# Kernel tuning notes

Hardware: AMD Instinct MI355X
Metric: run time of the kernel (lower is better)

The kernel has to match this reference:

```python
import jax, jax.numpy as jnp
import numpy as np

BN_EPS = 1e-5


def _posit_intervals():
    # Replicates conditions_l1 / conditions_g1 interval tables (128 steps each).
    l1, g1 = [], []
    for e in range(16):
        for j in range(8):
            if j == 0:
                l1.append((0.0, 1.0625 / 2**16, 1.0 / 2**16))
            else:
                lo = (1.0625 + 0.125 * (j - 1)) / 2 ** (16 - e)
                hi = (1.0625 + 0.125 * j) / 2 ** (16 - e)
                l1.append((lo, hi, 0.5 * (lo + hi)))
            lo = (1.0625 + 0.125 * (j - 1)) * 2 ** e
            hi = (1.0625 + 0.125 * j) * 2 ** e
            g1.append((lo, hi, 0.5 * (lo + hi)))  # note: j==8 branch in torch code is dead
    return l1, g1

_L1, _G1 = _posit_intervals()


def posit_quantize(x):
    # Faithful emulation of the 128 sequential torch.where passes.
    ax = jnp.abs(x)          # conditions are fixed from the ORIGINAL tensor
    neg = x < 0
    y = x
    for (lo1, hi1, m1), (log_, hig, mg) in zip(_L1, _G1):
        c1 = jnp.logical_and(ax > lo1, ax < hi1)
        cg = jnp.logical_and(ax > log_, ax < hig)
        v1 = jnp.where(neg, -m1, m1).astype(x.dtype)
        vg = jnp.where(neg, -mg, mg).astype(x.dtype)
        # |y| < 1 gate uses the CURRENT tensor, as in the torch loop
        y = jnp.where(jnp.abs(y) < 1, jnp.where(c1, v1, y), jnp.where(cg, vg, y))
    return y


def conv1x1(x, w, b):
    # x: [N,C,D,H,W], w: [O,C] (kernel_size=1), b: [O]
    return jnp.einsum('ncdhw,oc->nodhw', x, w) + b[None, :, None, None, None]


def batchnorm(x, gamma, beta, mean, var):
    inv = gamma / jnp.sqrt(var + BN_EPS)
    return x * inv[None, :, None, None, None] + (beta - mean * inv)[None, :, None, None, None]


def setup_inputs() -> dict:
    key = jax.random.key(0)
    ks = jax.random.split(key, 12)
    C = 256
    x = jax.random.normal(ks[0], (8, C, 16, 32, 32), dtype=jnp.float32)
    w1 = jax.random.normal(ks[1], (C, C), dtype=jnp.float32) * 0.05
    b1 = jax.random.normal(ks[2], (C,), dtype=jnp.float32) * 0.05
    w2 = jax.random.normal(ks[3], (C, C), dtype=jnp.float32) * 0.05
    b2 = jax.random.normal(ks[4], (C,), dtype=jnp.float32) * 0.05
    g1 = jax.random.uniform(ks[5], (C,)) + 0.5
    be1 = jax.random.normal(ks[6], (C,)) * 0.1
    m1 = jax.random.normal(ks[7], (C,)) * 0.1
    v1 = jax.random.uniform(ks[8], (C,)) + 0.5
    g2 = jax.random.uniform(ks[9], (C,)) + 0.5
    be2 = jax.random.normal(ks[10], (C,)) * 0.1
    m2 = jax.random.normal(ks[11], (C,)) * 0.1
    v2 = jax.random.uniform(jax.random.fold_in(key, 99), (C,)) + 0.5
    return {"x": x, "w1": w1, "b1": b1, "g1": g1, "be1": be1, "m1": m1, "v1": v1,
            "w2": w2, "b2": b2, "g2": g2, "be2": be2, "m2": m2, "v2": v2}


def reference(x, w1, b1, g1, be1, m1, v1, w2, b2, g2, be2, m2, v2):
    residual = x
    out = conv1x1(posit_quantize(x), posit_quantize(w1), b1)
    out = jax.nn.relu(batchnorm(out, g1, be1, m1, v1))
    out = conv1x1(posit_quantize(out), posit_quantize(w2), b2)
    out = batchnorm(out, g2, be2, m2, v2)
    return jax.nn.relu(out + residual)
```

## Files before the change

### kernel.cpp

```cpp
#include <hip/hip_runtime.h>

typedef __attribute__((ext_vector_type(8))) short short8;
typedef __attribute__((ext_vector_type(4))) short s4v;
typedef __attribute__((ext_vector_type(4))) float floatx4;

#define SPOS 16384

__device__ __forceinline__ unsigned short f2bf(float f) {
    unsigned u = __float_as_uint(f);
    u += 0x7fffu + ((u >> 16) & 1u);
    return (unsigned short)(u >> 16);
}

__device__ __forceinline__ float posit_q(float x) {
    unsigned xu  = __float_as_uint(x);
    unsigned sgn = xu & 0x80000000u;
    unsigned au  = xu & 0x7fffffffu;
    unsigned m   = au & 0x007fffffu;
    unsigned r   = (au + 0x00080000u) & 0xfff00000u;
    bool bdry = (m & 0x000fffffu) == 0x00080000u;
    unsigned res;
    if (au >= 0x3f800000u) {
        res = r;
        if (m > 0x00700000u && m < 0x00780000u && au < 0x47700000u)
            res = (au & 0xff800000u) + 0x00800000u;
        if ((bdry && m != 0x00780000u) || au >= 0x47780000u)
            res = au;
    } else {
        res = (m <= 0x00080000u || m >= 0x00780000u || bdry) ? au : r;
        if (au < 0x37880000u) res = au ? 0x37800000u : 0u;
    }
    return __uint_as_float(sgn | res);
}

__global__ __launch_bounds__(256) void prep_kernel(
    const float* __restrict__ w1, const float* __restrict__ w2,
    const float* __restrict__ b1, const float* __restrict__ g1,
    const float* __restrict__ be1, const float* __restrict__ m1,
    const float* __restrict__ v1,
    const float* __restrict__ b2, const float* __restrict__ g2,
    const float* __restrict__ be2, const float* __restrict__ m2,
    const float* __restrict__ v2,
    unsigned short* __restrict__ w1q, unsigned short* __restrict__ w2q,
    float* __restrict__ cst)
{
    int i = blockIdx.x * 256 + threadIdx.x;
    if (i < 65536) {
        w1q[i] = f2bf(posit_q(w1[i]));
        w2q[i] = f2bf(posit_q(w2[i]));
        if (i < 256) {
            float inv1 = g1[i] / sqrtf(v1[i] + 1e-5f);
            cst[i]       = inv1;
            cst[256 + i] = fmaf(b1[i], inv1, be1[i] - m1[i] * inv1);
            float inv2 = g2[i] / sqrtf(v2[i] + 1e-5f);
            cst[512 + i] = inv2;
            cst[768 + i] = fmaf(b2[i], inv2, be2[i] - m2[i] * inv2);
        }
    }
}

__device__ __forceinline__ int qidx(int p, int cb) {
    return p * 256 + ((cb ^ (p & 31)) << 3);
}

__global__ __launch_bounds__(256, 4) void fused_kernel(
    const float* __restrict__ x,
    const unsigned short* __restrict__ w1q,
    const unsigned short* __restrict__ w2q,
    const float* __restrict__ cst,
    float* __restrict__ out)
{
    __shared__ alignas(16) unsigned short q[64 * 256];
    __shared__ alignas(16) float xs[4 * 512];

    const int b  = blockIdx.x;
    const int n  = b >> 8;
    const int s0 = (b & 255) << 6;
    const float* xb = x   + (size_t)n * (256 * SPOS) + s0;
    float*       ob = out + (size_t)n * (256 * SPOS) + s0;

    const int t    = threadIdx.x;
    const int lane = t & 63;
    const int w    = t >> 6;
    const int quad = lane >> 4;
    const int l15  = lane & 15;

    {
        const int g  = lane & 15;
        const int co = lane >> 4;
        float* xsw = xs + w * 512;
        const float* src0 = xb + (size_t)(64 * w + co) * SPOS + 4 * g;
        #pragma unroll
        for (int r = 0; r < 8; ++r) {
            const float4 v0 = *(const float4*)(src0 + (size_t)(8 * r) * SPOS);
            const float4 v1 = *(const float4*)(src0 + (size_t)(8 * r + 4) * SPOS);
            *(float4*)&xsw[co * 64 + ((4 * g) ^ (4 * co))]             = v0;
            *(float4*)&xsw[(co + 4) * 64 + ((4 * g) ^ (4 * (co + 4)))] = v1;
            short8 pk;
            #pragma unroll
            for (int c8 = 0; c8 < 8; ++c8)
                pk[c8] = (short)f2bf(posit_q(xsw[c8 * 64 + (lane ^ (4 * c8))]));
            *(short8*)&q[qidx(lane, 8 * w + r)] = pk;
        }
    }
    __syncthreads();

    const int mbase = w * 64;
    floatx4 acc[4][4];
    #pragma unroll
    for (int i = 0; i < 4; ++i)
        #pragma unroll
        for (int jj = 0; jj < 4; ++jj)
            acc[i][jj] = (floatx4)0.0f;

    #pragma unroll
    for (int kk = 0; kk < 256; kk += 32) {
        short8 af[4], bf[4];
        #pragma unroll
        for (int i = 0; i < 4; ++i)
            af[i] = *(const short8*)&w1q[(size_t)(mbase + 16 * i + l15) * 256 + kk + quad * 8];
        #pragma unroll
        for (int jj = 0; jj < 4; ++jj)
            bf[jj] = *(const short8*)&q[qidx(16 * jj + l15, (kk >> 3) + quad)];
        #pragma unroll
        for (int i = 0; i < 4; ++i)
            #pragma unroll
            for (int jj = 0; jj < 4; ++jj)
                acc[i][jj] = __builtin_amdgcn_mfma_f32_16x16x32_bf16(af[i], bf[jj], acc[i][jj], 0, 0, 0);
    }
    __syncthreads();

    {
        const float* sc1 = cst;
        const float* bi1 = cst + 256;
        #pragma unroll
        for (int i = 0; i < 4; ++i) {
            const int m0 = mbase + 16 * i + quad * 4;
            float sc[4], bi[4];
            #pragma unroll
            for (int r = 0; r < 4; ++r) { sc[r] = sc1[m0 + r]; bi[r] = bi1[m0 + r]; }
            #pragma unroll
            for (int jj = 0; jj < 4; ++jj) {
                const int p = 16 * jj + l15;
                s4v h;
                #pragma unroll
                for (int r = 0; r < 4; ++r) {
                    float z = fmaf(acc[i][jj][r], sc[r], bi[r]);
                    z = fmaxf(z, 0.0f);
                    h[r] = (short)f2bf(posit_q(z));
                }
                *(s4v*)&q[qidx(p, m0 >> 3) + (m0 & 7)] = h;
            }
        }
    }
    __syncthreads();

    #pragma unroll
    for (int i = 0; i < 4; ++i)
        #pragma unroll
        for (int jj = 0; jj < 4; ++jj)
            acc[i][jj] = (floatx4)0.0f;

    #pragma unroll
    for (int kk = 0; kk < 256; kk += 32) {
        short8 af[4], bf[4];
        #pragma unroll
        for (int i = 0; i < 4; ++i)
            af[i] = *(const short8*)&w2q[(size_t)(mbase + 16 * i + l15) * 256 + kk + quad * 8];
        #pragma unroll
        for (int jj = 0; jj < 4; ++jj)
            bf[jj] = *(const short8*)&q[qidx(16 * jj + l15, (kk >> 3) + quad)];
        #pragma unroll
        for (int i = 0; i < 4; ++i)
            #pragma unroll
            for (int jj = 0; jj < 4; ++jj)
                acc[i][jj] = __builtin_amdgcn_mfma_f32_16x16x32_bf16(af[i], bf[jj], acc[i][jj], 0, 0, 0);
    }

    {
        const float* sc2 = cst + 512;
        const float* bi2 = cst + 768;
        #pragma unroll
        for (int i = 0; i < 4; ++i) {
            const int m0 = mbase + 16 * i + quad * 4;
            float sc[4], bi[4];
            #pragma unroll
            for (int r = 0; r < 4; ++r) { sc[r] = sc2[m0 + r]; bi[r] = bi2[m0 + r]; }
            #pragma unroll
            for (int jj = 0; jj < 4; ++jj) {
                const int p = 16 * jj + l15;
                #pragma unroll
                for (int r = 0; r < 4; ++r) {
                    const size_t off = (size_t)(m0 + r) * SPOS + p;
                    float v = fmaf(acc[i][jj][r], sc[r], bi[r]);
                    v += xb[off];
                    ob[off] = fmaxf(v, 0.0f);
                }
            }
        }
    }
}

extern "C" void kernel_launch(void* const* d_in, const int* in_sizes, int n_in,
                              void* d_out, int out_size, void* d_ws, size_t ws_size,
                              hipStream_t stream) {
    const float* x   = (const float*)d_in[0];
    const float* w1  = (const float*)d_in[1];
    const float* b1  = (const float*)d_in[2];
    const float* g1  = (const float*)d_in[3];
    const float* be1 = (const float*)d_in[4];
    const float* m1  = (const float*)d_in[5];
    const float* v1  = (const float*)d_in[6];
    const float* w2  = (const float*)d_in[7];
    const float* b2  = (const float*)d_in[8];
    const float* g2  = (const float*)d_in[9];
    const float* be2 = (const float*)d_in[10];
    const float* m2  = (const float*)d_in[11];
    const float* v2  = (const float*)d_in[12];

    unsigned short* w1q = (unsigned short*)d_ws;
    unsigned short* w2q = w1q + 65536;
    float* cst = (float*)(w2q + 65536);

    prep_kernel<<<256, 256, 0, stream>>>(w1, w2, b1, g1, be1, m1, v1,
                                         b2, g2, be2, m2, v2, w1q, w2q, cst);
    fused_kernel<<<2048, 256, 0, stream>>>(x, w1q, w2q, cst, (float*)d_out);
}
```

Measured before the change: 365.7 us.

## Halve spatial tile to 32 positions per block and raise occupancy

Each block now covers 32 spatial positions instead of 64, so the grid doubles to 4096 blocks. Shared memory for the activation tile and the staging buffer shrinks, the accumulator array halves, and launch bounds ask for 5 blocks per CU. The staging and transpose indexing and the swizzle are rewritten to fit the narrower tile, and a sign-free posit quantizer is used after the ReLU. The aim is more resident waves to hide memory latency, at the cost of loading the weight fragments twice as often per output and writing shorter 128-byte rows to global memory.

```diff
diff --git a/kernel.cpp b/kernel.cpp
--- a/kernel.cpp
+++ b/kernel.cpp
@@ -31,6 +31,25 @@
         if (au < 0x37880000u) res = au ? 0x37800000u : 0u;
     }
     return __uint_as_float(sgn | res);
+}
+
+__device__ __forceinline__ float posit_q_pos(float z) {
+    unsigned au  = __float_as_uint(z);
+    unsigned m   = au & 0x007fffffu;
+    unsigned r   = (au + 0x00080000u) & 0xfff00000u;
+    bool bdry = (m & 0x000fffffu) == 0x00080000u;
+    unsigned res;
+    if (au >= 0x3f800000u) {
+        res = r;
+        if (m > 0x00700000u && m < 0x00780000u && au < 0x47700000u)
+            res = (au & 0xff800000u) + 0x00800000u;
+        if ((bdry && m != 0x00780000u) || au >= 0x47780000u)
+            res = au;
+    } else {
+        res = (m <= 0x00080000u || m >= 0x00780000u || bdry) ? au : r;
+        if (au < 0x37880000u) res = au ? 0x37800000u : 0u;
+    }
+    return __uint_as_float(res);
 }
 
 __global__ __launch_bounds__(256) void prep_kernel(
@@ -60,22 +79,22 @@
 }
 
 __device__ __forceinline__ int qidx(int p, int cb) {
-    return p * 256 + ((cb ^ (p & 31)) << 3);
-}
-
-__global__ __launch_bounds__(256, 4) void fused_kernel(
+    return p * 256 + (((cb ^ p) & 31) << 3);
+}
+
+__global__ __launch_bounds__(256, 5) void fused_kernel(
     const float* __restrict__ x,
     const unsigned short* __restrict__ w1q,
     const unsigned short* __restrict__ w2q,
     const float* __restrict__ cst,
     float* __restrict__ out)
 {
-    __shared__ alignas(16) unsigned short q[64 * 256];
-    __shared__ alignas(16) float xs[4 * 512];
+    __shared__ alignas(16) unsigned short q[32 * 256];
+    __shared__ alignas(16) float xs[4 * 256];
 
     const int b  = blockIdx.x;
-    const int n  = b >> 8;
-    const int s0 = (b & 255) << 6;
+    const int n  = b >> 9;
+    const int s0 = (b & 511) << 5;
     const float* xb = x   + (size_t)n * (256 * SPOS) + s0;
     float*       ob = out + (size_t)n * (256 * SPOS) + s0;
 
@@ -86,46 +105,49 @@
     const int l15  = lane & 15;
 
     {
-        const int g  = lane & 15;
-        const int co = lane >> 4;
-        float* xsw = xs + w * 512;
-        const float* src0 = xb + (size_t)(64 * w + co) * SPOS + 4 * g;
+        const int row  = lane >> 3;
+        const int g    = lane & 7;
+        const int p    = lane & 31;
+        const int half = lane >> 5;
+        float* xsw = xs + w * 256;
+        const float* src0 = xb + (size_t)(64 * w + row) * SPOS + 4 * g;
         #pragma unroll
         for (int r = 0; r < 8; ++r) {
-            const float4 v0 = *(const float4*)(src0 + (size_t)(8 * r) * SPOS);
-            const float4 v1 = *(const float4*)(src0 + (size_t)(8 * r + 4) * SPOS);
-            *(float4*)&xsw[co * 64 + ((4 * g) ^ (4 * co))]             = v0;
-            *(float4*)&xsw[(co + 4) * 64 + ((4 * g) ^ (4 * (co + 4)))] = v1;
-            short8 pk;
-            #pragma unroll
-            for (int c8 = 0; c8 < 8; ++c8)
-                pk[c8] = (short)f2bf(posit_q(xsw[c8 * 64 + (lane ^ (4 * c8))]));
-            *(short8*)&q[qidx(lane, 8 * w + r)] = pk;
+            const float4 v = *(const float4*)(src0 + (size_t)(8 * r) * SPOS);
+            *(float4*)&xsw[row * 32 + ((4 * g) ^ (4 * row))] = v;
+            s4v pk;
+            #pragma unroll
+            for (int j = 0; j < 4; ++j) {
+                const int cl = 4 * half + j;
+                pk[j] = (short)f2bf(posit_q(
+                    xsw[cl * 32 + (((p & 28) ^ (4 * cl)) | (p & 3))]));
+            }
+            *(s4v*)&q[qidx(p, 8 * w + r) + 4 * half] = pk;
         }
     }
     __syncthreads();
 
     const int mbase = w * 64;
-    floatx4 acc[4][4];
+    floatx4 acc[4][2];
     #pragma unroll
     for (int i = 0; i < 4; ++i)
         #pragma unroll
-        for (int jj = 0; jj < 4; ++jj)
+        for (int jj = 0; jj < 2; ++jj)
             acc[i][jj] = (floatx4)0.0f;
 
     #pragma unroll
     for (int kk = 0; kk < 256; kk += 32) {
-        short8 af[4], bf[4];
+        short8 af[4], bf[2];
         #pragma unroll
         for (int i = 0; i < 4; ++i)
             af[i] = *(const short8*)&w1q[(size_t)(mbase + 16 * i + l15) * 256 + kk + quad * 8];
         #pragma unroll
-        for (int jj = 0; jj < 4; ++jj)
+        for (int jj = 0; jj < 2; ++jj)
             bf[jj] = *(const short8*)&q[qidx(16 * jj + l15, (kk >> 3) + quad)];
         #pragma unroll
         for (int i = 0; i < 4; ++i)
             #pragma unroll
-            for (int jj = 0; jj < 4; ++jj)
+            for (int jj = 0; jj < 2; ++jj)
                 acc[i][jj] = __builtin_amdgcn_mfma_f32_16x16x32_bf16(af[i], bf[jj], acc[i][jj], 0, 0, 0);
     }
     __syncthreads();
@@ -140,14 +162,14 @@
             #pragma unroll
             for (int r = 0; r < 4; ++r) { sc[r] = sc1[m0 + r]; bi[r] = bi1[m0 + r]; }
             #pragma unroll
-            for (int jj = 0; jj < 4; ++jj) {
+            for (int jj = 0; jj < 2; ++jj) {
                 const int p = 16 * jj + l15;
                 s4v h;
                 #pragma unroll
                 for (int r = 0; r < 4; ++r) {
                     float z = fmaf(acc[i][jj][r], sc[r], bi[r]);
                     z = fmaxf(z, 0.0f);
-                    h[r] = (short)f2bf(posit_q(z));
+                    h[r] = (short)f2bf(posit_q_pos(z));
                 }
                 *(s4v*)&q[qidx(p, m0 >> 3) + (m0 & 7)] = h;
             }
@@ -158,22 +180,22 @@
     #pragma unroll
     for (int i = 0; i < 4; ++i)
         #pragma unroll
-        for (int jj = 0; jj < 4; ++jj)
+        for (int jj = 0; jj < 2; ++jj)
             acc[i][jj] = (floatx4)0.0f;
 
     #pragma unroll
     for (int kk = 0; kk < 256; kk += 32) {
-        short8 af[4], bf[4];
+        short8 af[4], bf[2];
         #pragma unroll
         for (int i = 0; i < 4; ++i)
             af[i] = *(const short8*)&w2q[(size_t)(mbase + 16 * i + l15) * 256 + kk + quad * 8];
         #pragma unroll
-        for (int jj = 0; jj < 4; ++jj)
+        for (int jj = 0; jj < 2; ++jj)
             bf[jj] = *(const short8*)&q[qidx(16 * jj + l15, (kk >> 3) + quad)];
         #pragma unroll
         for (int i = 0; i < 4; ++i)
             #pragma unroll
-            for (int jj = 0; jj < 4; ++jj)
+            for (int jj = 0; jj < 2; ++jj)
                 acc[i][jj] = __builtin_amdgcn_mfma_f32_16x16x32_bf16(af[i], bf[jj], acc[i][jj], 0, 0, 0);
     }
 
@@ -187,7 +209,7 @@
             #pragma unroll
             for (int r = 0; r < 4; ++r) { sc[r] = sc2[m0 + r]; bi[r] = bi2[m0 + r]; }
             #pragma unroll
-            for (int jj = 0; jj < 4; ++jj) {
+            for (int jj = 0; jj < 2; ++jj) {
                 const int p = 16 * jj + l15;
                 #pragma unroll
                 for (int r = 0; r < 4; ++r) {
@@ -224,5 +246,5 @@
 
     prep_kernel<<<256, 256, 0, stream>>>(w1, w2, b1, g1, be1, m1, v1,
                                          b2, g2, be2, m2, v2, w1q, w2q, cst);
-    fused_kernel<<<2048, 256, 0, stream>>>(x, w1q, w2q, cst, (float*)d_out);
-}
+    fused_kernel<<<4096, 256, 0, stream>>>(x, w1q, w2q, cst, (float*)d_out);
+}
```

After: 433.5 us. +18.5%, slower.

## Pre-pack weights into MFMA fragment order, batch x loads, prefetch w2 fragment

Applied to the files above, without the earlier changes.

Weights are repacked in the prep kernel so each lane's A-fragment is a contiguous 16-byte chunk, which makes the global weight loads fully coalesced. All 16 x float4 loads are issued up front into registers before the LDS transpose/quantize pass, and that pass uses a double-buffered staging area. The first w2 fragment is prefetched before the barrier, and a sign-free posit variant is used after the ReLU. Occupancy hint drops from 4 to 3 blocks and LDS per block grows, trading occupancy for more memory-level parallelism.

```diff
diff --git a/kernel.cpp b/kernel.cpp
--- a/kernel.cpp
+++ b/kernel.cpp
@@ -33,6 +33,25 @@
     return __uint_as_float(sgn | res);
 }
 
+__device__ __forceinline__ float posit_q_pos(float z) {
+    unsigned au  = __float_as_uint(z);
+    unsigned m   = au & 0x007fffffu;
+    unsigned r   = (au + 0x00080000u) & 0xfff00000u;
+    bool bdry = (m & 0x000fffffu) == 0x00080000u;
+    unsigned res;
+    if (au >= 0x3f800000u) {
+        res = r;
+        if (m > 0x00700000u && m < 0x00780000u && au < 0x47700000u)
+            res = (au & 0xff800000u) + 0x00800000u;
+        if ((bdry && m != 0x00780000u) || au >= 0x47780000u)
+            res = au;
+    } else {
+        res = (m <= 0x00080000u || m >= 0x00780000u || bdry) ? au : r;
+        if (au < 0x37880000u) res = au ? 0x37800000u : 0u;
+    }
+    return __uint_as_float(res);
+}
+
 __global__ __launch_bounds__(256) void prep_kernel(
     const float* __restrict__ w1, const float* __restrict__ w2,
     const float* __restrict__ b1, const float* __restrict__ g1,
@@ -41,13 +60,19 @@
     const float* __restrict__ b2, const float* __restrict__ g2,
     const float* __restrict__ be2, const float* __restrict__ m2,
     const float* __restrict__ v2,
-    unsigned short* __restrict__ w1q, unsigned short* __restrict__ w2q,
+    unsigned short* __restrict__ w1p, unsigned short* __restrict__ w2p,
     float* __restrict__ cst)
 {
     int i = blockIdx.x * 256 + threadIdx.x;
     if (i < 65536) {
-        w1q[i] = f2bf(posit_q(w1[i]));
-        w2q[i] = f2bf(posit_q(w2[i]));
+        const int j    = i & 7;
+        const int lane = (i >> 3) & 63;
+        const int kb   = (i >> 9) & 7;
+        const int G    = i >> 12;
+        const int row  = 16 * G + (lane & 15);
+        const int k    = 32 * kb + 8 * (lane >> 4) + j;
+        w1p[i] = f2bf(posit_q(w1[row * 256 + k]));
+        w2p[i] = f2bf(posit_q(w2[row * 256 + k]));
         if (i < 256) {
             float inv1 = g1[i] / sqrtf(v1[i] + 1e-5f);
             cst[i]       = inv1;
@@ -63,15 +88,15 @@
     return p * 256 + ((cb ^ (p & 31)) << 3);
 }
 
-__global__ __launch_bounds__(256, 4) void fused_kernel(
+__global__ __launch_bounds__(256, 3) void fused_kernel(
     const float* __restrict__ x,
-    const unsigned short* __restrict__ w1q,
-    const unsigned short* __restrict__ w2q,
+    const unsigned short* __restrict__ w1p,
+    const unsigned short* __restrict__ w2p,
     const float* __restrict__ cst,
     float* __restrict__ out)
 {
     __shared__ alignas(16) unsigned short q[64 * 256];
-    __shared__ alignas(16) float xs[4 * 512];
+    __shared__ alignas(16) float xs[4 * 1024];
 
     const int b  = blockIdx.x;
     const int n  = b >> 8;
@@ -88,24 +113,28 @@
     {
         const int g  = lane & 15;
         const int co = lane >> 4;
-        float* xsw = xs + w * 512;
+        float* xsw = xs + w * 1024;
         const float* src0 = xb + (size_t)(64 * w + co) * SPOS + 4 * g;
+        float4 v[16];
         #pragma unroll
         for (int r = 0; r < 8; ++r) {
-            const float4 v0 = *(const float4*)(src0 + (size_t)(8 * r) * SPOS);
-            const float4 v1 = *(const float4*)(src0 + (size_t)(8 * r + 4) * SPOS);
-            *(float4*)&xsw[co * 64 + ((4 * g) ^ (4 * co))]             = v0;
-            *(float4*)&xsw[(co + 4) * 64 + ((4 * g) ^ (4 * (co + 4)))] = v1;
+            v[2 * r]     = *(const float4*)(src0 + (size_t)(8 * r) * SPOS);
+            v[2 * r + 1] = *(const float4*)(src0 + (size_t)(8 * r + 4) * SPOS);
+        }
+        #pragma unroll
+        for (int r = 0; r < 8; ++r) {
+            float* xr = xsw + (r & 1) * 512;
+            *(float4*)&xr[co * 64 + ((4 * g) ^ (4 * co))]             = v[2 * r];
+            *(float4*)&xr[(co + 4) * 64 + ((4 * g) ^ (4 * (co + 4)))] = v[2 * r + 1];
             short8 pk;
             #pragma unroll
             for (int c8 = 0; c8 < 8; ++c8)
-                pk[c8] = (short)f2bf(posit_q(xsw[c8 * 64 + (lane ^ (4 * c8))]));
+                pk[c8] = (short)f2bf(posit_q(xr[c8 * 64 + (lane ^ (4 * c8))]));
             *(short8*)&q[qidx(lane, 8 * w + r)] = pk;
         }
     }
     __syncthreads();
 
-    const int mbase = w * 64;
     floatx4 acc[4][4];
     #pragma unroll
     for (int i = 0; i < 4; ++i)
@@ -118,7 +147,7 @@
         short8 af[4], bf[4];
         #pragma unroll
         for (int i = 0; i < 4; ++i)
-            af[i] = *(const short8*)&w1q[(size_t)(mbase + 16 * i + l15) * 256 + kk + quad * 8];
+            af[i] = *(const short8*)&w1p[(((w * 4 + i) * 8 + (kk >> 5)) * 64 + lane) * 8];
         #pragma unroll
         for (int jj = 0; jj < 4; ++jj)
             bf[jj] = *(const short8*)&q[qidx(16 * jj + l15, (kk >> 3) + quad)];
@@ -128,7 +157,15 @@
             for (int jj = 0; jj < 4; ++jj)
                 acc[i][jj] = __builtin_amdgcn_mfma_f32_16x16x32_bf16(af[i], bf[jj], acc[i][jj], 0, 0, 0);
     }
+
+    short8 af20[4];
+    #pragma unroll
+    for (int i = 0; i < 4; ++i)
+        af20[i] = *(const short8*)&w2p[(((w * 4 + i) * 8 + 0) * 64 + lane) * 8];
+
     __syncthreads();
+
+    const int mbase = w * 64;
 
     {
         const float* sc1 = cst;
@@ -147,7 +184,7 @@
                 for (int r = 0; r < 4; ++r) {
                     float z = fmaf(acc[i][jj][r], sc[r], bi[r]);
                     z = fmaxf(z, 0.0f);
-                    h[r] = (short)f2bf(posit_q(z));
+                    h[r] = (short)f2bf(posit_q_pos(z));
                 }
                 *(s4v*)&q[qidx(p, m0 >> 3) + (m0 & 7)] = h;
             }
@@ -166,7 +203,8 @@
         short8 af[4], bf[4];
         #pragma unroll
         for (int i = 0; i < 4; ++i)
-            af[i] = *(const short8*)&w2q[(size_t)(mbase + 16 * i + l15) * 256 + kk + quad * 8];
+            af[i] = (kk == 0) ? af20[i]
+                  : *(const short8*)&w2p[(((w * 4 + i) * 8 + (kk >> 5)) * 64 + lane) * 8];
         #pragma unroll
         for (int jj = 0; jj < 4; ++jj)
             bf[jj] = *(const short8*)&q[qidx(16 * jj + l15, (kk >> 3) + quad)];
@@ -218,11 +256,11 @@
     const float* m2  = (const float*)d_in[11];
     const float* v2  = (const float*)d_in[12];
 
-    unsigned short* w1q = (unsigned short*)d_ws;
-    unsigned short* w2q = w1q + 65536;
-    float* cst = (float*)(w2q + 65536);
+    unsigned short* w1p = (unsigned short*)d_ws;
+    unsigned short* w2p = w1p + 65536;
+    float* cst = (float*)(w2p + 65536);
 
     prep_kernel<<<256, 256, 0, stream>>>(w1, w2, b1, g1, be1, m1, v1,
-                                         b2, g2, be2, m2, v2, w1q, w2q, cst);
-    fused_kernel<<<2048, 256, 0, stream>>>(x, w1q, w2q, cst, (float*)d_out);
-}
+                                         b2, g2, be2, m2, v2, w1p, w2p, cst);
+    fused_kernel<<<2048, 256, 0, stream>>>(x, w1p, w2p, cst, (float*)d_out);
+}
```

After: 343.2 us. 6.1% less time.
